# Kernel tuning notes

Hardware: AMD Instinct MI355X
Metric: run time of the kernel (lower is better)

The kernel has to match this reference:

```python
import jax, jax.numpy as jnp
import numpy as np

BS = 128  # quantization block size


def _dequant(w, s, bs):
    # w: [E, O, I]; s: [E, O//bs, I//bs] block scales -> broadcast to full weight
    return w * jnp.repeat(jnp.repeat(s, bs, axis=1), bs, axis=2)


def setup_inputs() -> dict:
    key = jax.random.key(0)
    ks = jax.random.split(key, 9)
    T, H, I, E, K = 512, 2048, 1024, 16, 4
    x = jax.random.normal(ks[0], (T, H), dtype=jnp.float32)
    w0 = jax.random.normal(ks[1], (E, I, H), dtype=jnp.float32) * 0.02
    w1 = jax.random.normal(ks[2], (E, I, H), dtype=jnp.float32) * 0.02
    w2 = jax.random.normal(ks[3], (E, H, I), dtype=jnp.float32) * 0.02
    s0 = jax.random.uniform(ks[4], (E, I // BS, H // BS), dtype=jnp.float32) + 0.5
    s1 = jax.random.uniform(ks[5], (E, I // BS, H // BS), dtype=jnp.float32) + 0.5
    s2 = jax.random.uniform(ks[6], (E, H // BS, I // BS), dtype=jnp.float32) + 0.5
    selected_experts = jax.random.randint(ks[7], (T, K), 0, E, dtype=jnp.int64)
    routing_weights = jax.random.uniform(ks[8], (T, K), dtype=jnp.float32)
    return {"x": x, "w0": w0, "w1": w1, "w2": w2, "s0": s0, "s1": s1,
            "s2": s2, "selected_experts": selected_experts,
            "routing_weights": routing_weights}


def reference(x, w0, w1, w2, s0, s1, s2, selected_experts, routing_weights):
    # Dequantize block-quantized expert weights
    w0d = _dequant(w0, s0, BS)  # [E, I, H] gate proj
    w1d = _dequant(w1, s1, BS)  # [E, I, H] up proj
    w2d = _dequant(w2, s2, BS)  # [E, H, I] down proj
    # SwiGLU FFN for every (token, expert) pair via batched GEMMs
    g = jnp.einsum('th,eih->tei', x, w0d)          # [T, E, I]
    u = jnp.einsum('th,eih->tei', x, w1d)          # [T, E, I]
    h = jax.nn.silu(g) * u                          # [T, E, I]
    y = jnp.einsum('tei,ehi->teh', h, w2d)          # [T, E, H]
    # Gather the top-k selected experts per token and weight them
    idx = selected_experts[:, :, None]              # [T, K, 1]
    y_sel = jnp.take_along_axis(y, idx, axis=1)     # [T, K, H]
    out = y_sel * routing_weights[:, :, None]       # [T, K, H]
    return out
```

## Files before the change

### kernel.cpp

```cpp
#include <hip/hip_runtime.h>
#include <math.h>

#define T_DIM 512
#define H_DIM 2048
#define I_DIM 1024
#define E_DIM 16
#define NP    2048
#define PM    256
#define MAXCH 24
#define LIST_OFF 256
#define HWS_OFF  8192
#define BK    128
#define LDK   136

typedef float  float4v __attribute__((ext_vector_type(4)));
typedef short  short8v __attribute__((ext_vector_type(8)));

__device__ __forceinline__ unsigned int bfr(float f) {
    unsigned int u = __builtin_bit_cast(unsigned int, f);
    return (u + 0x7fffu + ((u >> 16) & 1u)) >> 16;
}
__device__ __forceinline__ unsigned int cvt2(float a, float b) {
    unsigned int r;
    asm("v_cvt_pk_bf16_f32 %0, %1, %2" : "=v"(r) : "v"(a), "v"(b));
    return r;
}

__global__ __launch_bounds__(1024) void route_kernel(const int* __restrict__ sel,
                                                     int* __restrict__ meta) {
    __shared__ int cnt[E_DIM];
    __shared__ int wptr[E_DIM];
    int tid = threadIdx.x;
    if (tid < E_DIM) cnt[tid] = 0;
    __syncthreads();
    int p0 = tid, p1 = tid + 1024;
    int e0 = sel[p0], e1 = sel[p1];
    atomicAdd(&cnt[e0], 1);
    atomicAdd(&cnt[e1], 1);
    for (int i = tid; i < MAXCH * PM; i += 1024) meta[LIST_OFF + i] = -1;
    __syncthreads();
    if (tid == 0) {
        int off = 0, ci = 0;
        for (int e = 0; e < E_DIM; ++e) {
            wptr[e] = off;
            int nch = (cnt[e] + PM - 1) / PM;
            for (int j = 0; j < nch; ++j) meta[32 + ci++] = e;
            off += nch * PM;
        }
        for (; ci < MAXCH; ++ci) meta[32 + ci] = -1;
    }
    __syncthreads();
    int pos0 = atomicAdd(&wptr[e0], 1);
    meta[LIST_OFF + pos0] = p0;
    int pos1 = atomicAdd(&wptr[e1], 1);
    meta[LIST_OFF + pos1] = p1;
}

__global__ __launch_bounds__(1024, 4) void gemm01_kernel(
    const float* __restrict__ x, const float* __restrict__ w0g,
    const float* __restrict__ w1g, const float* __restrict__ s0,
    const float* __restrict__ s1, const int* __restrict__ meta,
    unsigned short* __restrict__ hbuf) {
    int e = meta[32 + blockIdx.y];
    if (e < 0) return;
    int itile = blockIdx.x;
    int tid = threadIdx.x;

    __shared__ unsigned short xs[PM][LDK];
    __shared__ unsigned short as[64][LDK];
    __shared__ unsigned short bs[64][LDK];
    __shared__ int prow[PM];
    __shared__ int trow[PM];

    if (tid < PM) {
        int p = meta[LIST_OFF + blockIdx.y * PM + tid];
        prow[tid] = p;
        trow[tid] = p >= 0 ? (p >> 2) : 0;
    }
    __syncthreads();

    const int lane = tid & 63;
    const int wid  = tid >> 6;
    const int l15  = lane & 15;
    const int kq   = (lane >> 4) * 8;
    const int ib   = itile >> 1;

    float4v zero = {0.f, 0.f, 0.f, 0.f};
    float4v accg[4], accu[4];
#pragma unroll
    for (int t = 0; t < 4; ++t) { accg[t] = zero; accu[t] = zero; }

    const int rx = tid >> 2, cx = tid & 3;
    const int rw_ = tid >> 4, cw = tid & 15;
    const float* xrow  = x   + (size_t)trow[rx] * H_DIM + cx * 32;
    const float* w0row = w0g + ((size_t)e * I_DIM + itile * 64 + rw_) * H_DIM + cw * 8;
    const float* w1row = w1g + ((size_t)e * I_DIM + itile * 64 + rw_) * H_DIM + cw * 8;
    const float* s0p = s0 + ((size_t)e * (I_DIM/128) + ib) * (H_DIM/128);
    const float* s1p = s1 + ((size_t)e * (I_DIM/128) + ib) * (H_DIM/128);

    float4 px[8], pa0, pa1, pb0, pb1;
#pragma unroll
    for (int q = 0; q < 8; ++q) px[q] = *(const float4*)(xrow + q * 4);
    pa0 = *(const float4*)(w0row);
    pa1 = *(const float4*)(w0row + 4);
    pb0 = *(const float4*)(w1row);
    pb1 = *(const float4*)(w1row + 4);

    for (int hb = 0; hb < H_DIM / BK; ++hb) {
        float sg = s0p[hb];
        float su = s1p[hb];
#pragma unroll
        for (int j = 0; j < 4; ++j) {
            uint4 v = make_uint4(cvt2(px[2*j].x,   px[2*j].y),
                                 cvt2(px[2*j].z,   px[2*j].w),
                                 cvt2(px[2*j+1].x, px[2*j+1].y),
                                 cvt2(px[2*j+1].z, px[2*j+1].w));
            *(uint4*)&xs[rx][cx * 32 + j * 8] = v;
        }
        *(uint4*)&as[rw_][cw * 8] = make_uint4(
            cvt2(pa0.x * sg, pa0.y * sg), cvt2(pa0.z * sg, pa0.w * sg),
            cvt2(pa1.x * sg, pa1.y * sg), cvt2(pa1.z * sg, pa1.w * sg));
        *(uint4*)&bs[rw_][cw * 8] = make_uint4(
            cvt2(pb0.x * su, pb0.y * su), cvt2(pb0.z * su, pb0.w * su),
            cvt2(pb1.x * su, pb1.y * su), cvt2(pb1.z * su, pb1.w * su));
        __syncthreads();
        if (hb + 1 < H_DIM / BK) {
            const int h0 = (hb + 1) * BK;
#pragma unroll
            for (int q = 0; q < 8; ++q) px[q] = *(const float4*)(xrow + h0 + q * 4);
            pa0 = *(const float4*)(w0row + h0);
            pa1 = *(const float4*)(w0row + h0 + 4);
            pb0 = *(const float4*)(w1row + h0);
            pb1 = *(const float4*)(w1row + h0 + 4);
        }
#pragma unroll
        for (int ks = 0; ks < BK / 32; ++ks) {
            int koff = ks * 32 + kq;
            short8v af = *(const short8v*)&xs[wid * 16 + l15][koff];
#pragma unroll
            for (int nt = 0; nt < 4; ++nt) {
                short8v b0 = *(const short8v*)&as[nt * 16 + l15][koff];
                accg[nt] = __builtin_amdgcn_mfma_f32_16x16x32_bf16(af, b0, accg[nt], 0, 0, 0);
                short8v b1 = *(const short8v*)&bs[nt * 16 + l15][koff];
                accu[nt] = __builtin_amdgcn_mfma_f32_16x16x32_bf16(af, b1, accu[nt], 0, 0, 0);
            }
        }
        __syncthreads();
    }

    int rowb = wid * 16 + (lane >> 4) * 4;
    int colb = itile * 64 + l15;
#pragma unroll
    for (int nt = 0; nt < 4; ++nt) {
#pragma unroll
        for (int rg = 0; rg < 4; ++rg) {
            int p = prow[rowb + rg];
            if (p < 0) continue;
            float g = accg[nt][rg], u = accu[nt][rg];
            float h = g / (1.f + __expf(-g)) * u;
            hbuf[(size_t)p * I_DIM + colb + nt * 16] = (unsigned short)bfr(h);
        }
    }
}

__global__ __launch_bounds__(1024, 4) void gemm2_kernel(
    const unsigned short* __restrict__ hbuf, const float* __restrict__ w2g,
    const float* __restrict__ s2, const float* __restrict__ rw,
    const int* __restrict__ meta, float* __restrict__ out) {
    int e = meta[32 + blockIdx.y];
    if (e < 0) return;
    int htile = blockIdx.x;
    int tid = threadIdx.x;

    __shared__ unsigned short hs[PM][LDK];
    __shared__ unsigned short wsm[64][LDK];
    __shared__ int prow[PM];

    if (tid < PM) prow[tid] = meta[LIST_OFF + blockIdx.y * PM + tid];
    __syncthreads();

    const int lane = tid & 63;
    const int wid  = tid >> 6;
    const int l15  = lane & 15;
    const int kq   = (lane >> 4) * 8;
    const int hbk  = htile >> 1;

    float4v zero = {0.f, 0.f, 0.f, 0.f};
    float4v acc[4];
#pragma unroll
    for (int t = 0; t < 4; ++t) acc[t] = zero;

    const int rx = tid >> 2, cx = tid & 3;
    const int rw_ = tid >> 4, cw = tid & 15;
    int pr = prow[rx]; if (pr < 0) pr = 0;
    const unsigned short* hrow = hbuf + (size_t)pr * I_DIM + cx * 32;
    const float* wrow = w2g + ((size_t)e * H_DIM + htile * 64 + rw_) * I_DIM + cw * 8;
    const float* s2p = s2 + ((size_t)e * (H_DIM/128) + hbk) * (I_DIM/128);

    uint4  ph[2];
    float4 pw0, pw1;
    ph[0] = *(const uint4*)(hrow);
    ph[1] = *(const uint4*)(hrow + 8);
    uint4 ph2[2];
    ph2[0] = *(const uint4*)(hrow + 16);
    ph2[1] = *(const uint4*)(hrow + 24);
    pw0 = *(const float4*)(wrow);
    pw1 = *(const float4*)(wrow + 4);

    for (int ibk = 0; ibk < I_DIM / BK; ++ibk) {
        float sc = s2p[ibk];
        *(uint4*)&hs[rx][cx * 32]      = ph[0];
        *(uint4*)&hs[rx][cx * 32 + 8]  = ph[1];
        *(uint4*)&hs[rx][cx * 32 + 16] = ph2[0];
        *(uint4*)&hs[rx][cx * 32 + 24] = ph2[1];
        *(uint4*)&wsm[rw_][cw * 8] = make_uint4(
            cvt2(pw0.x * sc, pw0.y * sc), cvt2(pw0.z * sc, pw0.w * sc),
            cvt2(pw1.x * sc, pw1.y * sc), cvt2(pw1.z * sc, pw1.w * sc));
        __syncthreads();
        if (ibk + 1 < I_DIM / BK) {
            const int i0 = (ibk + 1) * BK;
            ph[0]  = *(const uint4*)(hrow + i0);
            ph[1]  = *(const uint4*)(hrow + i0 + 8);
            ph2[0] = *(const uint4*)(hrow + i0 + 16);
            ph2[1] = *(const uint4*)(hrow + i0 + 24);
            pw0 = *(const float4*)(wrow + i0);
            pw1 = *(const float4*)(wrow + i0 + 4);
        }
#pragma unroll
        for (int ks = 0; ks < BK / 32; ++ks) {
            int koff = ks * 32 + kq;
            short8v af = *(const short8v*)&hs[wid * 16 + l15][koff];
#pragma unroll
            for (int nt = 0; nt < 4; ++nt) {
                short8v bfv = *(const short8v*)&wsm[nt * 16 + l15][koff];
                acc[nt] = __builtin_amdgcn_mfma_f32_16x16x32_bf16(af, bfv, acc[nt], 0, 0, 0);
            }
        }
        __syncthreads();
    }

    int rowb = wid * 16 + (lane >> 4) * 4;
    int colb = htile * 64 + l15;
#pragma unroll
    for (int nt = 0; nt < 4; ++nt) {
#pragma unroll
        for (int rg = 0; rg < 4; ++rg) {
            int p = prow[rowb + rg];
            if (p < 0) continue;
            out[(size_t)p * H_DIM + colb + nt * 16] = acc[nt][rg] * rw[p];
        }
    }
}

extern "C" void kernel_launch(void* const* d_in, const int* in_sizes, int n_in,
                              void* d_out, int out_size, void* d_ws, size_t ws_size,
                              hipStream_t stream) {
    const float* x  = (const float*)d_in[0];
    const float* w0 = (const float*)d_in[1];
    const float* w1 = (const float*)d_in[2];
    const float* w2 = (const float*)d_in[3];
    const float* s0 = (const float*)d_in[4];
    const float* s1 = (const float*)d_in[5];
    const float* s2 = (const float*)d_in[6];
    const int* sel  = (const int*)d_in[7];
    const float* rw = (const float*)d_in[8];
    float* out = (float*)d_out;
    int* meta = (int*)d_ws;
    unsigned short* hbuf = (unsigned short*)((float*)d_ws + HWS_OFF);

    route_kernel<<<1, 1024, 0, stream>>>(sel, meta);
    gemm01_kernel<<<dim3(I_DIM / 64, MAXCH), 1024, 0, stream>>>(x, w0, w1, s0, s1, meta, hbuf);
    gemm2_kernel<<<dim3(H_DIM / 64, MAXCH), 1024, 0, stream>>>(hbuf, w2, s2, rw, meta, out);
}
```

Measured before the change: 447.1 us.

## Pre-convert x to bf16 once and widen gemm2 output tile to 128 columns

Adds a small kernel that converts x to bf16 once into workspace, so gemm01 loads half the bytes for the token tile and skips per-block conversion that every I-tile repeated. gemm2 now computes 128 H columns per block instead of 64, halving how often the gathered h rows are reloaded and making each block line up with one scale block. The cost is an extra kernel launch, more accumulator registers and LDS in gemm2, and half as many gemm2 blocks.

```diff
diff --git a/kernel.cpp b/kernel.cpp
--- a/kernel.cpp
+++ b/kernel.cpp
@@ -9,7 +9,8 @@
 #define PM    256
 #define MAXCH 24
 #define LIST_OFF 256
-#define HWS_OFF  8192
+#define XB_OFF   8192
+#define HWS_OFF  (XB_OFF + 524288)
 #define BK    128
 #define LDK   136
 
@@ -24,6 +25,19 @@
     unsigned int r;
     asm("v_cvt_pk_bf16_f32 %0, %1, %2" : "=v"(r) : "v"(a), "v"(b));
     return r;
+}
+
+__global__ __launch_bounds__(256) void xprep_kernel(const float* __restrict__ x,
+                                                    unsigned short* __restrict__ xb) {
+    int idx = (blockIdx.x * 256 + threadIdx.x) * 16;
+    float4 a = *(const float4*)(x + idx);
+    float4 b = *(const float4*)(x + idx + 4);
+    float4 c = *(const float4*)(x + idx + 8);
+    float4 d = *(const float4*)(x + idx + 12);
+    uint4 lo = make_uint4(cvt2(a.x, a.y), cvt2(a.z, a.w), cvt2(b.x, b.y), cvt2(b.z, b.w));
+    uint4 hi = make_uint4(cvt2(c.x, c.y), cvt2(c.z, c.w), cvt2(d.x, d.y), cvt2(d.z, d.w));
+    *(uint4*)(xb + idx) = lo;
+    *(uint4*)(xb + idx + 8) = hi;
 }
 
 __global__ __launch_bounds__(1024) void route_kernel(const int* __restrict__ sel,
@@ -57,7 +71,7 @@
 }
 
 __global__ __launch_bounds__(1024, 4) void gemm01_kernel(
-    const float* __restrict__ x, const float* __restrict__ w0g,
+    const unsigned short* __restrict__ xb, const float* __restrict__ w0g,
     const float* __restrict__ w1g, const float* __restrict__ s0,
     const float* __restrict__ s1, const int* __restrict__ meta,
     unsigned short* __restrict__ hbuf) {
@@ -92,15 +106,16 @@
 
     const int rx = tid >> 2, cx = tid & 3;
     const int rw_ = tid >> 4, cw = tid & 15;
-    const float* xrow  = x   + (size_t)trow[rx] * H_DIM + cx * 32;
+    const unsigned short* xrow = xb + (size_t)trow[rx] * H_DIM + cx * 32;
     const float* w0row = w0g + ((size_t)e * I_DIM + itile * 64 + rw_) * H_DIM + cw * 8;
     const float* w1row = w1g + ((size_t)e * I_DIM + itile * 64 + rw_) * H_DIM + cw * 8;
     const float* s0p = s0 + ((size_t)e * (I_DIM/128) + ib) * (H_DIM/128);
     const float* s1p = s1 + ((size_t)e * (I_DIM/128) + ib) * (H_DIM/128);
 
-    float4 px[8], pa0, pa1, pb0, pb1;
-#pragma unroll
-    for (int q = 0; q < 8; ++q) px[q] = *(const float4*)(xrow + q * 4);
+    uint4  px[4];
+    float4 pa0, pa1, pb0, pb1;
+#pragma unroll
+    for (int q = 0; q < 4; ++q) px[q] = *(const uint4*)(xrow + q * 8);
     pa0 = *(const float4*)(w0row);
     pa1 = *(const float4*)(w0row + 4);
     pb0 = *(const float4*)(w1row);
@@ -110,13 +125,8 @@
         float sg = s0p[hb];
         float su = s1p[hb];
 #pragma unroll
-        for (int j = 0; j < 4; ++j) {
-            uint4 v = make_uint4(cvt2(px[2*j].x,   px[2*j].y),
-                                 cvt2(px[2*j].z,   px[2*j].w),
-                                 cvt2(px[2*j+1].x, px[2*j+1].y),
-                                 cvt2(px[2*j+1].z, px[2*j+1].w));
-            *(uint4*)&xs[rx][cx * 32 + j * 8] = v;
-        }
+        for (int j = 0; j < 4; ++j)
+            *(uint4*)&xs[rx][cx * 32 + j * 8] = px[j];
         *(uint4*)&as[rw_][cw * 8] = make_uint4(
             cvt2(pa0.x * sg, pa0.y * sg), cvt2(pa0.z * sg, pa0.w * sg),
             cvt2(pa1.x * sg, pa1.y * sg), cvt2(pa1.z * sg, pa1.w * sg));
@@ -127,7 +137,7 @@
         if (hb + 1 < H_DIM / BK) {
             const int h0 = (hb + 1) * BK;
 #pragma unroll
-            for (int q = 0; q < 8; ++q) px[q] = *(const float4*)(xrow + h0 + q * 4);
+            for (int q = 0; q < 4; ++q) px[q] = *(const uint4*)(xrow + h0 + q * 8);
             pa0 = *(const float4*)(w0row + h0);
             pa1 = *(const float4*)(w0row + h0 + 4);
             pb0 = *(const float4*)(w1row + h0);
@@ -173,7 +183,7 @@
     int tid = threadIdx.x;
 
     __shared__ unsigned short hs[PM][LDK];
-    __shared__ unsigned short wsm[64][LDK];
+    __shared__ unsigned short wsm[128][LDK];
     __shared__ int prow[PM];
 
     if (tid < PM) prow[tid] = meta[LIST_OFF + blockIdx.y * PM + tid];
@@ -183,55 +193,53 @@
     const int wid  = tid >> 6;
     const int l15  = lane & 15;
     const int kq   = (lane >> 4) * 8;
-    const int hbk  = htile >> 1;
 
     float4v zero = {0.f, 0.f, 0.f, 0.f};
-    float4v acc[4];
-#pragma unroll
-    for (int t = 0; t < 4; ++t) acc[t] = zero;
+    float4v acc[8];
+#pragma unroll
+    for (int t = 0; t < 8; ++t) acc[t] = zero;
 
     const int rx = tid >> 2, cx = tid & 3;
-    const int rw_ = tid >> 4, cw = tid & 15;
+    const int rw_ = tid >> 3, cw = tid & 7;
     int pr = prow[rx]; if (pr < 0) pr = 0;
     const unsigned short* hrow = hbuf + (size_t)pr * I_DIM + cx * 32;
-    const float* wrow = w2g + ((size_t)e * H_DIM + htile * 64 + rw_) * I_DIM + cw * 8;
-    const float* s2p = s2 + ((size_t)e * (H_DIM/128) + hbk) * (I_DIM/128);
-
-    uint4  ph[2];
-    float4 pw0, pw1;
-    ph[0] = *(const uint4*)(hrow);
-    ph[1] = *(const uint4*)(hrow + 8);
-    uint4 ph2[2];
-    ph2[0] = *(const uint4*)(hrow + 16);
-    ph2[1] = *(const uint4*)(hrow + 24);
-    pw0 = *(const float4*)(wrow);
-    pw1 = *(const float4*)(wrow + 4);
+    const float* wrow = w2g + ((size_t)e * H_DIM + htile * 128 + rw_) * I_DIM + cw * 16;
+    const float* s2p = s2 + ((size_t)e * (H_DIM/128) + htile) * (I_DIM/128);
+
+    uint4  ph[4];
+    float4 pw[4];
+#pragma unroll
+    for (int q = 0; q < 4; ++q) {
+        ph[q] = *(const uint4*)(hrow + q * 8);
+        pw[q] = *(const float4*)(wrow + q * 4);
+    }
 
     for (int ibk = 0; ibk < I_DIM / BK; ++ibk) {
         float sc = s2p[ibk];
-        *(uint4*)&hs[rx][cx * 32]      = ph[0];
-        *(uint4*)&hs[rx][cx * 32 + 8]  = ph[1];
-        *(uint4*)&hs[rx][cx * 32 + 16] = ph2[0];
-        *(uint4*)&hs[rx][cx * 32 + 24] = ph2[1];
-        *(uint4*)&wsm[rw_][cw * 8] = make_uint4(
-            cvt2(pw0.x * sc, pw0.y * sc), cvt2(pw0.z * sc, pw0.w * sc),
-            cvt2(pw1.x * sc, pw1.y * sc), cvt2(pw1.z * sc, pw1.w * sc));
+#pragma unroll
+        for (int q = 0; q < 4; ++q)
+            *(uint4*)&hs[rx][cx * 32 + q * 8] = ph[q];
+        *(uint4*)&wsm[rw_][cw * 16] = make_uint4(
+            cvt2(pw[0].x * sc, pw[0].y * sc), cvt2(pw[0].z * sc, pw[0].w * sc),
+            cvt2(pw[1].x * sc, pw[1].y * sc), cvt2(pw[1].z * sc, pw[1].w * sc));
+        *(uint4*)&wsm[rw_][cw * 16 + 8] = make_uint4(
+            cvt2(pw[2].x * sc, pw[2].y * sc), cvt2(pw[2].z * sc, pw[2].w * sc),
+            cvt2(pw[3].x * sc, pw[3].y * sc), cvt2(pw[3].z * sc, pw[3].w * sc));
         __syncthreads();
         if (ibk + 1 < I_DIM / BK) {
             const int i0 = (ibk + 1) * BK;
-            ph[0]  = *(const uint4*)(hrow + i0);
-            ph[1]  = *(const uint4*)(hrow + i0 + 8);
-            ph2[0] = *(const uint4*)(hrow + i0 + 16);
-            ph2[1] = *(const uint4*)(hrow + i0 + 24);
-            pw0 = *(const float4*)(wrow + i0);
-            pw1 = *(const float4*)(wrow + i0 + 4);
+#pragma unroll
+            for (int q = 0; q < 4; ++q) {
+                ph[q] = *(const uint4*)(hrow + i0 + q * 8);
+                pw[q] = *(const float4*)(wrow + i0 + q * 4);
+            }
         }
 #pragma unroll
         for (int ks = 0; ks < BK / 32; ++ks) {
             int koff = ks * 32 + kq;
             short8v af = *(const short8v*)&hs[wid * 16 + l15][koff];
 #pragma unroll
-            for (int nt = 0; nt < 4; ++nt) {
+            for (int nt = 0; nt < 8; ++nt) {
                 short8v bfv = *(const short8v*)&wsm[nt * 16 + l15][koff];
                 acc[nt] = __builtin_amdgcn_mfma_f32_16x16x32_bf16(af, bfv, acc[nt], 0, 0, 0);
             }
@@ -240,9 +248,9 @@
     }
 
     int rowb = wid * 16 + (lane >> 4) * 4;
-    int colb = htile * 64 + l15;
-#pragma unroll
-    for (int nt = 0; nt < 4; ++nt) {
+    int colb = htile * 128 + l15;
+#pragma unroll
+    for (int nt = 0; nt < 8; ++nt) {
 #pragma unroll
         for (int rg = 0; rg < 4; ++rg) {
             int p = prow[rowb + rg];
@@ -266,9 +274,11 @@
     const float* rw = (const float*)d_in[8];
     float* out = (float*)d_out;
     int* meta = (int*)d_ws;
+    unsigned short* xb   = (unsigned short*)((float*)d_ws + XB_OFF);
     unsigned short* hbuf = (unsigned short*)((float*)d_ws + HWS_OFF);
 
+    xprep_kernel<<<256, 256, 0, stream>>>(x, xb);
     route_kernel<<<1, 1024, 0, stream>>>(sel, meta);
-    gemm01_kernel<<<dim3(I_DIM / 64, MAXCH), 1024, 0, stream>>>(x, w0, w1, s0, s1, meta, hbuf);
-    gemm2_kernel<<<dim3(H_DIM / 64, MAXCH), 1024, 0, stream>>>(hbuf, w2, s2, rw, meta, out);
-}
+    gemm01_kernel<<<dim3(I_DIM / 64, MAXCH), 1024, 0, stream>>>(xb, w0, w1, s0, s1, meta, hbuf);
+    gemm2_kernel<<<dim3(H_DIM / 128, MAXCH), 1024, 0, stream>>>(hbuf, w2, s2, rw, meta, out);
+}
```

New measurement: 506.2 us. 13.2% more time.

## Double-buffer LDS tiles with K=64 in both expert GEMM kernels

Applied to the files above, without the earlier changes.

Both GEMM kernels now use two shared-memory buffers with a K tile of 64 instead of a single buffer with a K tile of 128. The next tile is loaded from global memory and written into the alternate buffer while MFMAs run on the current one, which removes one __syncthreads per iteration. A sched_barrier keeps the global loads issued ahead of the MFMA block. The trade-off is twice as many iterations with less MFMA work per barrier, and half as many bytes loaded per thread per step.

```diff
diff --git a/kernel.cpp b/kernel.cpp
--- a/kernel.cpp
+++ b/kernel.cpp
@@ -10,8 +10,8 @@
 #define MAXCH 24
 #define LIST_OFF 256
 #define HWS_OFF  8192
-#define BK    128
-#define LDK   136
+#define BK2   64
+#define LDB   72
 
 typedef float  float4v __attribute__((ext_vector_type(4)));
 typedef short  short8v __attribute__((ext_vector_type(8)));
@@ -66,9 +66,9 @@
     int itile = blockIdx.x;
     int tid = threadIdx.x;
 
-    __shared__ unsigned short xs[PM][LDK];
-    __shared__ unsigned short as[64][LDK];
-    __shared__ unsigned short bs[64][LDK];
+    __shared__ unsigned short xs[2][PM][LDB];
+    __shared__ unsigned short as_[2][64][LDB];
+    __shared__ unsigned short bs_[2][64][LDB];
     __shared__ int prow[PM];
     __shared__ int trow[PM];
 
@@ -91,61 +91,69 @@
     for (int t = 0; t < 4; ++t) { accg[t] = zero; accu[t] = zero; }
 
     const int rx = tid >> 2, cx = tid & 3;
-    const int rw_ = tid >> 4, cw = tid & 15;
-    const float* xrow  = x   + (size_t)trow[rx] * H_DIM + cx * 32;
-    const float* w0row = w0g + ((size_t)e * I_DIM + itile * 64 + rw_) * H_DIM + cw * 8;
-    const float* w1row = w1g + ((size_t)e * I_DIM + itile * 64 + rw_) * H_DIM + cw * 8;
+    const int rww = tid >> 4, cw = tid & 15;
+    const float* xrow  = x   + (size_t)trow[rx] * H_DIM + cx * 16;
+    const float* w0row = w0g + ((size_t)e * I_DIM + itile * 64 + rww) * H_DIM + cw * 4;
+    const float* w1row = w1g + ((size_t)e * I_DIM + itile * 64 + rww) * H_DIM + cw * 4;
     const float* s0p = s0 + ((size_t)e * (I_DIM/128) + ib) * (H_DIM/128);
     const float* s1p = s1 + ((size_t)e * (I_DIM/128) + ib) * (H_DIM/128);
 
-    float4 px[8], pa0, pa1, pb0, pb1;
-#pragma unroll
-    for (int q = 0; q < 8; ++q) px[q] = *(const float4*)(xrow + q * 4);
-    pa0 = *(const float4*)(w0row);
-    pa1 = *(const float4*)(w0row + 4);
-    pb0 = *(const float4*)(w1row);
-    pb1 = *(const float4*)(w1row + 4);
-
-    for (int hb = 0; hb < H_DIM / BK; ++hb) {
-        float sg = s0p[hb];
-        float su = s1p[hb];
-#pragma unroll
-        for (int j = 0; j < 4; ++j) {
-            uint4 v = make_uint4(cvt2(px[2*j].x,   px[2*j].y),
-                                 cvt2(px[2*j].z,   px[2*j].w),
-                                 cvt2(px[2*j+1].x, px[2*j+1].y),
-                                 cvt2(px[2*j+1].z, px[2*j+1].w));
-            *(uint4*)&xs[rx][cx * 32 + j * 8] = v;
-        }
-        *(uint4*)&as[rw_][cw * 8] = make_uint4(
-            cvt2(pa0.x * sg, pa0.y * sg), cvt2(pa0.z * sg, pa0.w * sg),
-            cvt2(pa1.x * sg, pa1.y * sg), cvt2(pa1.z * sg, pa1.w * sg));
-        *(uint4*)&bs[rw_][cw * 8] = make_uint4(
-            cvt2(pb0.x * su, pb0.y * su), cvt2(pb0.z * su, pb0.w * su),
-            cvt2(pb1.x * su, pb1.y * su), cvt2(pb1.z * su, pb1.w * su));
-        __syncthreads();
-        if (hb + 1 < H_DIM / BK) {
-            const int h0 = (hb + 1) * BK;
-#pragma unroll
-            for (int q = 0; q < 8; ++q) px[q] = *(const float4*)(xrow + h0 + q * 4);
-            pa0 = *(const float4*)(w0row + h0);
-            pa1 = *(const float4*)(w0row + h0 + 4);
-            pb0 = *(const float4*)(w1row + h0);
-            pb1 = *(const float4*)(w1row + h0 + 4);
-        }
-#pragma unroll
-        for (int ks = 0; ks < BK / 32; ++ks) {
+    float4 px[4], pa, pb;
+#pragma unroll
+    for (int q = 0; q < 4; ++q) px[q] = *(const float4*)(xrow + q * 4);
+    pa = *(const float4*)(w0row);
+    pb = *(const float4*)(w1row);
+    {
+        float sg = s0p[0], su = s1p[0];
+#pragma unroll
+        for (int j = 0; j < 2; ++j)
+            *(uint4*)&xs[0][rx][cx * 16 + j * 8] = make_uint4(
+                cvt2(px[2*j].x, px[2*j].y),   cvt2(px[2*j].z, px[2*j].w),
+                cvt2(px[2*j+1].x, px[2*j+1].y), cvt2(px[2*j+1].z, px[2*j+1].w));
+        *(uint2*)&as_[0][rww][cw * 4] = make_uint2(cvt2(pa.x * sg, pa.y * sg),
+                                                   cvt2(pa.z * sg, pa.w * sg));
+        *(uint2*)&bs_[0][rww][cw * 4] = make_uint2(cvt2(pb.x * su, pb.y * su),
+                                                   cvt2(pb.z * su, pb.w * su));
+    }
+    __syncthreads();
+
+    const int NT = H_DIM / BK2;
+    int cur = 0;
+    for (int t = 0; t < NT; ++t) {
+        if (t + 1 < NT) {
+            const int h0 = (t + 1) * BK2;
+#pragma unroll
+            for (int q = 0; q < 4; ++q) px[q] = *(const float4*)(xrow + h0 + q * 4);
+            pa = *(const float4*)(w0row + h0);
+            pb = *(const float4*)(w1row + h0);
+        }
+        __builtin_amdgcn_sched_barrier(0);
+#pragma unroll
+        for (int ks = 0; ks < BK2 / 32; ++ks) {
             int koff = ks * 32 + kq;
-            short8v af = *(const short8v*)&xs[wid * 16 + l15][koff];
+            short8v af = *(const short8v*)&xs[cur][wid * 16 + l15][koff];
 #pragma unroll
             for (int nt = 0; nt < 4; ++nt) {
-                short8v b0 = *(const short8v*)&as[nt * 16 + l15][koff];
+                short8v b0 = *(const short8v*)&as_[cur][nt * 16 + l15][koff];
                 accg[nt] = __builtin_amdgcn_mfma_f32_16x16x32_bf16(af, b0, accg[nt], 0, 0, 0);
-                short8v b1 = *(const short8v*)&bs[nt * 16 + l15][koff];
+                short8v b1 = *(const short8v*)&bs_[cur][nt * 16 + l15][koff];
                 accu[nt] = __builtin_amdgcn_mfma_f32_16x16x32_bf16(af, b1, accu[nt], 0, 0, 0);
             }
         }
+        if (t + 1 < NT) {
+            float sg = s0p[(t + 1) >> 1], su = s1p[(t + 1) >> 1];
+#pragma unroll
+            for (int j = 0; j < 2; ++j)
+                *(uint4*)&xs[cur ^ 1][rx][cx * 16 + j * 8] = make_uint4(
+                    cvt2(px[2*j].x, px[2*j].y),   cvt2(px[2*j].z, px[2*j].w),
+                    cvt2(px[2*j+1].x, px[2*j+1].y), cvt2(px[2*j+1].z, px[2*j+1].w));
+            *(uint2*)&as_[cur ^ 1][rww][cw * 4] = make_uint2(cvt2(pa.x * sg, pa.y * sg),
+                                                             cvt2(pa.z * sg, pa.w * sg));
+            *(uint2*)&bs_[cur ^ 1][rww][cw * 4] = make_uint2(cvt2(pb.x * su, pb.y * su),
+                                                             cvt2(pb.z * su, pb.w * su));
+        }
         __syncthreads();
+        cur ^= 1;
     }
 
     int rowb = wid * 16 + (lane >> 4) * 4;
@@ -172,8 +180,8 @@
     int htile = blockIdx.x;
     int tid = threadIdx.x;
 
-    __shared__ unsigned short hs[PM][LDK];
-    __shared__ unsigned short wsm[64][LDK];
+    __shared__ unsigned short hs[2][PM][LDB];
+    __shared__ unsigned short wsm[2][64][LDB];
     __shared__ int prow[PM];
 
     if (tid < PM) prow[tid] = meta[LIST_OFF + blockIdx.y * PM + tid];
@@ -191,52 +199,55 @@
     for (int t = 0; t < 4; ++t) acc[t] = zero;
 
     const int rx = tid >> 2, cx = tid & 3;
-    const int rw_ = tid >> 4, cw = tid & 15;
+    const int rww = tid >> 4, cw = tid & 15;
     int pr = prow[rx]; if (pr < 0) pr = 0;
-    const unsigned short* hrow = hbuf + (size_t)pr * I_DIM + cx * 32;
-    const float* wrow = w2g + ((size_t)e * H_DIM + htile * 64 + rw_) * I_DIM + cw * 8;
+    const unsigned short* hrow = hbuf + (size_t)pr * I_DIM + cx * 16;
+    const float* wrow = w2g + ((size_t)e * H_DIM + htile * 64 + rww) * I_DIM + cw * 4;
     const float* s2p = s2 + ((size_t)e * (H_DIM/128) + hbk) * (I_DIM/128);
 
     uint4  ph[2];
-    float4 pw0, pw1;
+    float4 pw;
     ph[0] = *(const uint4*)(hrow);
     ph[1] = *(const uint4*)(hrow + 8);
-    uint4 ph2[2];
-    ph2[0] = *(const uint4*)(hrow + 16);
-    ph2[1] = *(const uint4*)(hrow + 24);
-    pw0 = *(const float4*)(wrow);
-    pw1 = *(const float4*)(wrow + 4);
-
-    for (int ibk = 0; ibk < I_DIM / BK; ++ibk) {
-        float sc = s2p[ibk];
-        *(uint4*)&hs[rx][cx * 32]      = ph[0];
-        *(uint4*)&hs[rx][cx * 32 + 8]  = ph[1];
-        *(uint4*)&hs[rx][cx * 32 + 16] = ph2[0];
-        *(uint4*)&hs[rx][cx * 32 + 24] = ph2[1];
-        *(uint4*)&wsm[rw_][cw * 8] = make_uint4(
-            cvt2(pw0.x * sc, pw0.y * sc), cvt2(pw0.z * sc, pw0.w * sc),
-            cvt2(pw1.x * sc, pw1.y * sc), cvt2(pw1.z * sc, pw1.w * sc));
-        __syncthreads();
-        if (ibk + 1 < I_DIM / BK) {
-            const int i0 = (ibk + 1) * BK;
-            ph[0]  = *(const uint4*)(hrow + i0);
-            ph[1]  = *(const uint4*)(hrow + i0 + 8);
-            ph2[0] = *(const uint4*)(hrow + i0 + 16);
-            ph2[1] = *(const uint4*)(hrow + i0 + 24);
-            pw0 = *(const float4*)(wrow + i0);
-            pw1 = *(const float4*)(wrow + i0 + 4);
-        }
-#pragma unroll
-        for (int ks = 0; ks < BK / 32; ++ks) {
+    pw = *(const float4*)(wrow);
+    {
+        float sc = s2p[0];
+        *(uint4*)&hs[0][rx][cx * 16]     = ph[0];
+        *(uint4*)&hs[0][rx][cx * 16 + 8] = ph[1];
+        *(uint2*)&wsm[0][rww][cw * 4] = make_uint2(cvt2(pw.x * sc, pw.y * sc),
+                                                   cvt2(pw.z * sc, pw.w * sc));
+    }
+    __syncthreads();
+
+    const int NT2 = I_DIM / BK2;
+    int cur = 0;
+    for (int t = 0; t < NT2; ++t) {
+        if (t + 1 < NT2) {
+            const int i0 = (t + 1) * BK2;
+            ph[0] = *(const uint4*)(hrow + i0);
+            ph[1] = *(const uint4*)(hrow + i0 + 8);
+            pw = *(const float4*)(wrow + i0);
+        }
+        __builtin_amdgcn_sched_barrier(0);
+#pragma unroll
+        for (int ks = 0; ks < BK2 / 32; ++ks) {
             int koff = ks * 32 + kq;
-            short8v af = *(const short8v*)&hs[wid * 16 + l15][koff];
+            short8v af = *(const short8v*)&hs[cur][wid * 16 + l15][koff];
 #pragma unroll
             for (int nt = 0; nt < 4; ++nt) {
-                short8v bfv = *(const short8v*)&wsm[nt * 16 + l15][koff];
+                short8v bfv = *(const short8v*)&wsm[cur][nt * 16 + l15][koff];
                 acc[nt] = __builtin_amdgcn_mfma_f32_16x16x32_bf16(af, bfv, acc[nt], 0, 0, 0);
             }
         }
+        if (t + 1 < NT2) {
+            float sc = s2p[(t + 1) >> 1];
+            *(uint4*)&hs[cur ^ 1][rx][cx * 16]     = ph[0];
+            *(uint4*)&hs[cur ^ 1][rx][cx * 16 + 8] = ph[1];
+            *(uint2*)&wsm[cur ^ 1][rww][cw * 4] = make_uint2(cvt2(pw.x * sc, pw.y * sc),
+                                                             cvt2(pw.z * sc, pw.w * sc));
+        }
         __syncthreads();
+        cur ^= 1;
     }
 
     int rowb = wid * 16 + (lane >> 4) * 4;
```

Measured after the change: 420.5 us. 1.06x faster.
